# Optimization experiments

Measured on AMD Instinct MI355X. Metric: run time of the kernel, lower is better.

Reference implementation:

```python
import jax, jax.numpy as jnp
import numpy as np

EPS = 1e-4  # performer softmax-kernel stabilizer
LN_EPS = 1e-5


def _layernorm(x, g, b):
    m = jnp.mean(x, axis=-1, keepdims=True)
    v = jnp.mean(jnp.square(x - m), axis=-1, keepdims=True)
    return (x - m) * jax.lax.rsqrt(v + LN_EPS) * g + b


def _softmax_features(x, proj, is_query):
    # FAVOR+ positive softmax-kernel features. x: [B,H,N,Dh], proj: [M,Dh]
    d = x.shape[-1]
    xn = x * (d ** -0.25)                      # data normalizer d^{-1/4}
    u = jnp.einsum('bhnd,md->bhnm', xn, proj)  # [B,H,N,M]
    diag = 0.5 * jnp.sum(jnp.square(xn), axis=-1, keepdims=True)
    if is_query:
        stab = jnp.max(u, axis=-1, keepdims=True)
    else:
        stab = jnp.max(u, axis=(-2, -1), keepdims=True)
    ratio = proj.shape[0] ** -0.5
    return ratio * (jnp.exp(u - diag - stab) + EPS)


def reference(x, proj, ln1_g, ln1_b, ln2_g, ln2_b, W1, b1, W2, b2):
    B, N, E = x.shape
    M, Dh = proj.shape
    H = E // Dh

    # --- multi-head fast attention sublayer (pre-LN, q=k=v, no dropout) ---
    h = _layernorm(x, ln1_g, ln1_b)
    qkv = h.reshape(B, N, H, Dh).transpose(0, 2, 1, 3)     # [B,H,N,Dh]
    q_p = _softmax_features(qkv, proj, is_query=True)      # [B,H,N,M]
    k_p = _softmax_features(qkv, proj, is_query=False)     # [B,H,N,M]

    # non-causal linear attention: O(N*M*Dh)
    k_sum = jnp.sum(k_p, axis=-2)                          # [B,H,M]
    d_inv = 1.0 / jnp.einsum('bhnm,bhm->bhn', q_p, k_sum)  # [B,H,N]
    ctx = jnp.einsum('bhnm,bhnd->bhmd', k_p, qkv)          # [B,H,M,Dh]
    attn = jnp.einsum('bhnm,bhmd,bhn->bhnd', q_p, ctx, d_inv)
    attn = attn.transpose(0, 2, 1, 3).reshape(B, N, E)
    x = x + attn

    # --- MLP sublayer (pre-LN, GELU, dropout off in eval) ---
    h2 = _layernorm(x, ln2_g, ln2_b)
    h2 = jax.nn.gelu(h2 @ W1 + b1, approximate=False) @ W2 + b2
    return x + h2


def setup_inputs() -> dict:
    B, N, E, H, M, F = 4, 2048, 768, 12, 256, 3072
    Dh = E // H
    key = jax.random.key(0)
    ks = jax.random.split(key, 4)
    return {
        'x': jax.random.normal(ks[0], (B, N, E), jnp.float32),
        'proj': jax.random.normal(ks[1], (M, Dh), jnp.float32),
        'ln1_g': jnp.ones((E,), jnp.float32),
        'ln1_b': jnp.zeros((E,), jnp.float32),
        'ln2_g': jnp.ones((E,), jnp.float32),
        'ln2_b': jnp.zeros((E,), jnp.float32),
        'W1': jax.random.normal(ks[2], (E, F), jnp.float32) * 0.02,
        'b1': jnp.zeros((F,), jnp.float32),
        'W2': jax.random.normal(ks[3], (F, E), jnp.float32) * 0.02,
        'b2': jnp.zeros((E,), jnp.float32),
    }
```

## Files before the change

### kernel.cpp

```cpp
#include <hip/hip_runtime.h>
#include <hip/hip_bf16.h>
#include <math.h>

#define B_    4
#define N_    2048
#define E_    768
#define H_    12
#define M_    256
#define F_    3072
#define DH_   64
#define BN_   (B_ * N_)
#define BH_   (B_ * H_)
#define NSP_  16

#define EPS_F     1e-4f
#define LN_EPS_F  1e-5f
#define DNORM_F   0.35355339059327373f
#define DIAGC_F   0.0625f

typedef __attribute__((ext_vector_type(8))) short bf16x8;
typedef __attribute__((ext_vector_type(4))) float f32x4;

static __device__ __forceinline__ float to_f32(float v) { return v; }
static __device__ __forceinline__ float to_f32(__hip_bfloat16 v) { return __bfloat162float(v); }
static __device__ __forceinline__ short f2bf(float v) {
    __hip_bfloat16 b = __float2bfloat16(v);
    return *reinterpret_cast<short*>(&b);
}

static __device__ __forceinline__ float fast_gelu(float x) {
    float xc = fminf(fmaxf(x, -9.f), 9.f);
    float y = 0.7978845608028654f * (xc + 0.044715f * xc * xc * xc);
    float tt = __expf(-2.f * y);
    return x * __builtin_amdgcn_rcpf(1.f + tt);
}

static __device__ __forceinline__ void gld_lds16(const void* g, void* lds) {
    __builtin_amdgcn_global_load_lds((const __attribute__((address_space(1))) void*)g,
                                     (__attribute__((address_space(3))) void*)lds, 16, 0, 0);
}

__global__ void probe_kernel(const unsigned int* __restrict__ g1, int* __restrict__ flag) {
    if (threadIdx.x == 0 && blockIdx.x == 0)
        *flag = (*g1 == 0x3F803F80u) ? 1 : 0;
}

__global__ void convert_kernel(const void* __restrict__ src, __hip_bfloat16* __restrict__ dst,
                               int n, const int* __restrict__ flag) {
    int isb = *flag;
    int i = blockIdx.x * blockDim.x + threadIdx.x;
    int stride = gridDim.x * blockDim.x;
    if (isb) {
        const unsigned short* s = (const unsigned short*)src;
        unsigned short* d = (unsigned short*)dst;
        for (; i < n; i += stride) d[i] = s[i];
    } else {
        const float* s = (const float*)src;
        for (; i < n; i += stride) dst[i] = __float2bfloat16(s[i]);
    }
}

__global__ void convert_transpose_kernel(const void* __restrict__ src,
                                         __hip_bfloat16* __restrict__ dst,
                                         int R, int C, const int* __restrict__ flag) {
    __shared__ __hip_bfloat16 tile[32][33];
    int isb = *flag;
    int c0 = blockIdx.x * 32, r0 = blockIdx.y * 32;
    int tx = threadIdx.x & 31, ty = threadIdx.x >> 5;
    if (isb) {
        const unsigned short* s = (const unsigned short*)src;
        for (int j = 0; j < 4; ++j) {
            int r = ty + j * 8;
            ((unsigned short*)&tile[r][tx])[0] = s[(size_t)(r0 + r) * C + c0 + tx];
        }
    } else {
        const float* s = (const float*)src;
        for (int j = 0; j < 4; ++j) {
            int r = ty + j * 8;
            tile[r][tx] = __float2bfloat16(s[(size_t)(r0 + r) * C + c0 + tx]);
        }
    }
    __syncthreads();
    for (int j = 0; j < 4; ++j) {
        int r = ty + j * 8;
        dst[(size_t)(c0 + r) * R + r0 + tx] = tile[tx][r];
    }
}

template <typename TIn>
__global__ void ln_kernel(const TIn* __restrict__ x,
                          const __hip_bfloat16* __restrict__ g,
                          const __hip_bfloat16* __restrict__ b,
                          __hip_bfloat16* __restrict__ hout,
                          float* __restrict__ diag ) {
    int row = blockIdx.x;
    int t = threadIdx.x;
    __shared__ float rs[256], rq[256];
    __shared__ float hrow[E_];

    float xv[3];
    const TIn* xr = x + (size_t)row * E_;
    float s = 0.f, q = 0.f;
    for (int i = 0; i < 3; ++i) {
        xv[i] = to_f32(xr[t + i * 256]);
        s += xv[i];
        q += xv[i] * xv[i];
    }
    rs[t] = s; rq[t] = q;
    __syncthreads();
    for (int off = 128; off > 0; off >>= 1) {
        if (t < off) { rs[t] += rs[t + off]; rq[t] += rq[t + off]; }
        __syncthreads();
    }
    float mean = rs[0] * (1.0f / E_);
    float var  = rq[0] * (1.0f / E_) - mean * mean;
    float rinv = rsqrtf(fmaxf(var, 0.0f) + LN_EPS_F);

    __hip_bfloat16* hr = hout + (size_t)row * E_;
    for (int i = 0; i < 3; ++i) {
        int e = t + i * 256;
        float hv = (xv[i] - mean) * rinv * __bfloat162float(g[e]) + __bfloat162float(b[e]);
        hr[e] = __float2bfloat16(hv);
        hrow[e] = hv;
    }
    if (diag != nullptr) {
        __syncthreads();
        if (t < H_) {
            float acc = 0.f;
            for (int k = 0; k < DH_; ++k) { float v = hrow[t * DH_ + k]; acc += v * v; }
            diag[row * H_ + t] = DIAGC_F * acc;
        }
    }
}

__global__ __launch_bounds__(256) void ctx_mfma_kernel(
        const __hip_bfloat16* __restrict__ h,
        const __hip_bfloat16* __restrict__ proj,
        const float* __restrict__ diag,
        float* __restrict__ pctx, float* __restrict__ pksum,
        float* __restrict__ pmax, float* __restrict__ pvsum) {
    int sp = blockIdx.x, bh = blockIdx.y;
    int bb = bh / H_, hh = bh % H_;
    int n0 = sp * 128;
    int t = threadIdx.x, lane = t & 63, w = t >> 6;
    int lm = lane & 15, kg = lane >> 4;

    __shared__ __align__(16) short hv_s[128 * 72];
    __shared__ __align__(16) short vt_s[64 * 136];
    __shared__ __align__(16) short p_s[64 * 72];
    __shared__ __align__(16) short kpt_s[64 * 136];
    __shared__ float ksp_s[4][64];
    __shared__ float dg_s[128];
    __shared__ float wmax_s[4];
    __shared__ float vp_s[4][64];

    for (int it = 0; it < 4; ++it) {
        int c = t + it * 256; int n = c >> 3, kb = c & 7;
        uint4 vld = *(const uint4*)&h[((size_t)(bb * N_ + n0 + n)) * E_ + hh * DH_ + kb * 8];
        *(uint4*)&hv_s[n * 72 + kb * 8] = vld;
        union { uint4 u4; short sh[8]; } uu; uu.u4 = vld;
        for (int j = 0; j < 8; ++j) vt_s[(kb * 8 + j) * 136 + n] = uu.sh[j];
    }
    if (t < 128) dg_s[t] = diag[(size_t)(bb * N_ + n0 + t) * H_ + hh];
    __syncthreads();

    {
        int d = t & 63, rg = t >> 6;
        float s = 0.f;
        for (int n = rg * 32; n < rg * 32 + 32; ++n)
            s += __bfloat162float(*(const __hip_bfloat16*)&hv_s[n * 72 + d]);
        vp_s[rg][d] = s;
    }
    __syncthreads();
    if (t < 64)
        pvsum[((size_t)sp * BH_ + bh) * 64 + t] =
            vp_s[0][t] + vp_s[1][t] + vp_s[2][t] + vp_s[3][t];

    for (int q = 0; q < 4; ++q) {
        __syncthreads();
        for (int it = 0; it < 2; ++it) {
            int c = t + it * 256; int m = c >> 3, kb = c & 7;
            *(uint4*)&p_s[m * 72 + kb * 8] = *(const uint4*)&proj[(size_t)(q * 64 + m) * DH_ + kb * 8];
        }
        __syncthreads();

        f32x4 u[2][4];
        for (int i = 0; i < 2; ++i) for (int j = 0; j < 4; ++j) u[i][j] = (f32x4){0.f,0.f,0.f,0.f};
        for (int kc = 0; kc < 2; ++kc) {
            bf16x8 af[2], bf[4];
            for (int i = 0; i < 2; ++i)
                af[i] = *(const bf16x8*)&hv_s[(w * 32 + i * 16 + lm) * 72 + kc * 32 + kg * 8];
            for (int j = 0; j < 4; ++j)
                bf[j] = *(const bf16x8*)&p_s[(j * 16 + lm) * 72 + kc * 32 + kg * 8];
            for (int i = 0; i < 2; ++i)
                for (int j = 0; j < 4; ++j)
                    u[i][j] = __builtin_amdgcn_mfma_f32_16x16x32_bf16(af[i], bf[j], u[i][j], 0, 0, 0);
        }
        float lmax = -1e30f;
        for (int i = 0; i < 2; ++i) for (int j = 0; j < 4; ++j) for (int r = 0; r < 4; ++r) {
            u[i][j][r] *= DNORM_F;
            lmax = fmaxf(lmax, u[i][j][r]);
        }
        for (int off = 32; off >= 1; off >>= 1) lmax = fmaxf(lmax, __shfl_xor(lmax, off));
        if (lane == 0) wmax_s[w] = lmax;
        __syncthreads();
        float Lmax = fmaxf(fmaxf(wmax_s[0], wmax_s[1]), fmaxf(wmax_s[2], wmax_s[3]));

        float kpart[4] = {0.f, 0.f, 0.f, 0.f};
        for (int i = 0; i < 2; ++i) {
            float dgv[4];
            for (int r = 0; r < 4; ++r) dgv[r] = dg_s[w * 32 + i * 16 + kg * 4 + r];
            for (int j = 0; j < 4; ++j)
                for (int r = 0; r < 4; ++r) {
                    float val = expf(u[i][j][r] - dgv[r] - Lmax);
                    kpart[j] += val;
                    kpt_s[(j * 16 + lm) * 136 + (w * 32 + i * 16 + kg * 4 + r)] = f2bf(val);
                }
        }
        for (int j = 0; j < 4; ++j) {
            kpart[j] += __shfl_xor(kpart[j], 16);
            kpart[j] += __shfl_xor(kpart[j], 32);
        }
        if (lane < 16)
            for (int j = 0; j < 4; ++j) ksp_s[w][j * 16 + lm] = kpart[j];
        __syncthreads();

        f32x4 c4[4];
        for (int jd = 0; jd < 4; ++jd) c4[jd] = (f32x4){0.f,0.f,0.f,0.f};
        for (int kc = 0; kc < 4; ++kc) {
            bf16x8 a = *(const bf16x8*)&kpt_s[(w * 16 + lm) * 136 + kc * 32 + kg * 8];
            for (int jd = 0; jd < 4; ++jd) {
                bf16x8 b = *(const bf16x8*)&vt_s[(jd * 16 + lm) * 136 + kc * 32 + kg * 8];
                c4[jd] = __builtin_amdgcn_mfma_f32_16x16x32_bf16(a, b, c4[jd], 0, 0, 0);
            }
        }
        size_t base = ((size_t)sp * BH_ + bh) * M_ + q * 64 + w * 16;
        for (int jd = 0; jd < 4; ++jd)
            for (int r = 0; r < 4; ++r)
                pctx[(base + kg * 4 + r) * DH_ + jd * 16 + lm] = c4[jd][r];
        if (t < 64)
            pksum[((size_t)sp * BH_ + bh) * M_ + q * 64 + t] =
                ksp_s[0][t] + ksp_s[1][t] + ksp_s[2][t] + ksp_s[3][t];
        if (t == 0) pmax[bh * 64 + sp * 4 + q] = Lmax;
    }
}

__global__ void ctx_reduce_kernel(const float* __restrict__ pctx,
                                  const float* __restrict__ pksum,
                                  const float* __restrict__ pmax,
                                  const float* __restrict__ pvsum,
                                  __hip_bfloat16* __restrict__ ctx_t,
                                  float* __restrict__ ksum) {
    int mb = blockIdx.x, bh = blockIdx.y;
    int t = threadIdx.x;
    __shared__ float hm_s;
    __shared__ float sc_s[16];
    __shared__ float vs_s[64];
    __shared__ float tr_s[64 * 65];
    if (t < 64) {
        float v = pmax[bh * 64 + t];
        for (int off = 32; off >= 1; off >>= 1) v = fmaxf(v, __shfl_xor(v, off));
        if (t == 0) hm_s = v;
        float s = 0.f;
        for (int sp = 0; sp < 16; ++sp) s += pvsum[((size_t)sp * BH_ + bh) * 64 + t];
        vs_s[t] = s;
    }
    __syncthreads();
    if (t < 16) sc_s[t] = expf(pmax[bh * 64 + t * 4 + mb] - hm_s);
    __syncthreads();
    float scl[16];
    for (int sp = 0; sp < 16; ++sp) scl[sp] = sc_s[sp];
    int d = t & 63;
    for (int it = 0; it < 16; ++it) {
        int ml = (t >> 6) + it * 4;
        float acc = 0.f;
        for (int sp = 0; sp < 16; ++sp)
            acc += scl[sp] * pctx[(((size_t)sp * BH_ + bh) * M_ + mb * 64 + ml) * DH_ + d];
        tr_s[ml * 65 + d] = acc + EPS_F * vs_s[d];
    }
    if (t < 64) {
        float ka = 0.f;
        for (int sp = 0; sp < 16; ++sp)
            ka += scl[sp] * pksum[((size_t)sp * BH_ + bh) * M_ + mb * 64 + t];
        ksum[bh * M_ + mb * 64 + t] = ka + EPS_F * (float)N_;
    }
    __syncthreads();
    int mcol = t & 63;
    for (int jt = 0; jt < 16; ++jt) {
        int dl = (t >> 6) + jt * 4;
        ctx_t[((size_t)bh * DH_ + dl) * M_ + mb * 64 + mcol] = __float2bfloat16(tr_s[mcol * 65 + dl]);
    }
}

__global__ void sums_kernel(const __hip_bfloat16* __restrict__ ctx_t,
                            const float* __restrict__ ksum,
                            float* __restrict__ ctxsum, float* __restrict__ kssum) {
    int bh = blockIdx.x, t = threadIdx.x;
    __shared__ float red[256];
    int d = t >> 2, part = t & 3;
    float s = 0.f;
    for (int mm = part * 64; mm < part * 64 + 64; ++mm)
        s += __bfloat162float(ctx_t[((size_t)bh * DH_ + d) * M_ + mm]);
    red[t] = s;
    __syncthreads();
    if (t < 64) ctxsum[bh * 64 + t] = red[t * 4] + red[t * 4 + 1] + red[t * 4 + 2] + red[t * 4 + 3];
    __syncthreads();
    red[t] = ksum[bh * M_ + t];
    __syncthreads();
    for (int off = 128; off > 0; off >>= 1) {
        if (t < off) red[t] += red[t + off];
        __syncthreads();
    }
    if (t == 0) kssum[bh] = red[0];
}

__global__ __launch_bounds__(256) void attn_mfma_kernel(
        const __hip_bfloat16* __restrict__ h,
        const __hip_bfloat16* __restrict__ proj,
        const float* __restrict__ diag,
        const __hip_bfloat16* __restrict__ ctx_t,
        const float* __restrict__ ksum,
        const float* __restrict__ ctxsum,
        const float* __restrict__ kssum,
        const __hip_bfloat16* __restrict__ xin,
        float* __restrict__ x2) {
    int ntile = blockIdx.x, bh = blockIdx.y;
    int bb = bh / H_, hh = bh % H_;
    int n0 = ntile * 128;
    int t = threadIdx.x, lane = t & 63, w = t >> 6;
    int lm = lane & 15, kg = lane >> 4;

    __shared__ __align__(16) short hq_s[128 * 72];
    __shared__ __align__(16) short p_s[64 * 72];
    __shared__ __align__(16) short ct_s[64 * 72];
    __shared__ __align__(16) short qp_s[128 * 72];
    __shared__ float ksum_s[256];
    __shared__ float dg_s[128];
    __shared__ float cs_s[64];
    __shared__ float kss_s;

    for (int it = 0; it < 4; ++it) {
        int c = t + it * 256; int n = c >> 3, kb = c & 7;
        *(uint4*)&hq_s[n * 72 + kb * 8] =
            *(const uint4*)&h[((size_t)(bb * N_ + n0 + n)) * E_ + hh * DH_ + kb * 8];
    }
    if (t < 128) dg_s[t] = diag[(size_t)(bb * N_ + n0 + t) * H_ + hh];
    ksum_s[t] = ksum[bh * M_ + t];
    if (t < 64) cs_s[t] = ctxsum[bh * 64 + t];
    if (t == 0) kss_s = kssum[bh];

    f32x4 o[2][4];
    float qs[2][4], mrun[2][4];
    for (int i = 0; i < 2; ++i)
        for (int jd = 0; jd < 4; ++jd) o[i][jd] = (f32x4){0.f,0.f,0.f,0.f};
    for (int i = 0; i < 2; ++i)
        for (int r = 0; r < 4; ++r) { qs[i][r] = 0.f; mrun[i][r] = -1e30f; }

    for (int mc = 0; mc < 4; ++mc) {
        __syncthreads();
        for (int it = 0; it < 2; ++it) {
            int c = t + it * 256; int m = c >> 3, kb = c & 7;
            *(uint4*)&p_s[m * 72 + kb * 8] = *(const uint4*)&proj[(size_t)(mc * 64 + m) * DH_ + kb * 8];
            *(uint4*)&ct_s[m * 72 + kb * 8] =
                *(const uint4*)&ctx_t[((size_t)bh * DH_ + m) * M_ + mc * 64 + kb * 8];
        }
        __syncthreads();

        f32x4 u[2][4];
        for (int i = 0; i < 2; ++i) for (int j = 0; j < 4; ++j) u[i][j] = (f32x4){0.f,0.f,0.f,0.f};
        for (int kc = 0; kc < 2; ++kc) {
            bf16x8 af[2], bf[4];
            for (int i = 0; i < 2; ++i)
                af[i] = *(const bf16x8*)&hq_s[(w * 32 + i * 16 + lm) * 72 + kc * 32 + kg * 8];
            for (int j = 0; j < 4; ++j)
                bf[j] = *(const bf16x8*)&p_s[(j * 16 + lm) * 72 + kc * 32 + kg * 8];
            for (int i = 0; i < 2; ++i)
                for (int j = 0; j < 4; ++j)
                    u[i][j] = __builtin_amdgcn_mfma_f32_16x16x32_bf16(af[i], bf[j], u[i][j], 0, 0, 0);
        }
        for (int i = 0; i < 2; ++i) for (int j = 0; j < 4; ++j)
            for (int r = 0; r < 4; ++r) u[i][j][r] *= DNORM_F;

        for (int i = 0; i < 2; ++i)
            for (int r = 0; r < 4; ++r) {
                float cm = fmaxf(fmaxf(u[i][0][r], u[i][1][r]), fmaxf(u[i][2][r], u[i][3][r]));
                for (int off = 8; off >= 1; off >>= 1) cm = fmaxf(cm, __shfl_xor(cm, off));
                float mnew = fmaxf(mrun[i][r], cm);
                float sc = expf(mrun[i][r] - mnew);
                mrun[i][r] = mnew;
                qs[i][r] *= sc;
                for (int jd = 0; jd < 4; ++jd) o[i][jd][r] *= sc;
            }
        for (int i = 0; i < 2; ++i) {
            float dgv[4];
            for (int r = 0; r < 4; ++r) dgv[r] = dg_s[w * 32 + i * 16 + kg * 4 + r];
            for (int j = 0; j < 4; ++j) {
                float ksv = ksum_s[mc * 64 + j * 16 + lm];
                for (int r = 0; r < 4; ++r) {
                    float val = expf(u[i][j][r] - dgv[r] - mrun[i][r]);
                    qs[i][r] += val * ksv;
                    qp_s[(w * 32 + i * 16 + kg * 4 + r) * 72 + j * 16 + lm] = f2bf(val);
                }
            }
        }
        __syncthreads();
        for (int kc = 0; kc < 2; ++kc) {
            bf16x8 af[2], bf[4];
            for (int i = 0; i < 2; ++i)
                af[i] = *(const bf16x8*)&qp_s[(w * 32 + i * 16 + lm) * 72 + kc * 32 + kg * 8];
            for (int jd = 0; jd < 4; ++jd)
                bf[jd] = *(const bf16x8*)&ct_s[(jd * 16 + lm) * 72 + kc * 32 + kg * 8];
            for (int i = 0; i < 2; ++i)
                for (int jd = 0; jd < 4; ++jd)
                    o[i][jd] = __builtin_amdgcn_mfma_f32_16x16x32_bf16(af[i], bf[jd], o[i][jd], 0, 0, 0);
        }
    }

    for (int i = 0; i < 2; ++i)
        for (int r = 0; r < 4; ++r)
            for (int off = 8; off >= 1; off >>= 1) qs[i][r] += __shfl_xor(qs[i][r], off);
    float kss = kss_s;
    for (int i = 0; i < 2; ++i)
        for (int r = 0; r < 4; ++r) {
            float dinv = 1.0f / (qs[i][r] + EPS_F * kss);
            size_t row = (size_t)(bb * N_ + n0 + w * 32 + i * 16 + kg * 4 + r);
            for (int jd = 0; jd < 4; ++jd) {
                int dcol = jd * 16 + lm;
                float outv = (o[i][jd][r] + EPS_F * cs_s[dcol]) * dinv;
                int col = hh * DH_ + dcol;
                x2[row * E_ + col] = __bfloat162float(xin[row * E_ + col]) + outv;
            }
        }
}

template <int KK, int NCOLS, bool DO_GELU>
__global__ __launch_bounds__(256, 2) void mfma_mlp_kernel(
        const __hip_bfloat16* __restrict__ A,
        const __hip_bfloat16* __restrict__ Bt,
        const __hip_bfloat16* __restrict__ bias,
        const float* __restrict__ resid,
        void* __restrict__ outv,
        const int* __restrict__ oflag) {
    constexpr int TM = 128, TN = 128;
    constexpr int CA = TM / 16;
    constexpr int CPS = CA + TN / 16;
    constexpr int CPW = CPS / 4;
    constexpr int LBUF = CPS * 512;
    constexpr int NT = KK / 32;
    constexpr int NXB = NCOLS / TN;
    constexpr int NWG = NXB * (BN_ / TM);
    constexpr int CPX = NWG / 8;

    const int t = threadIdx.x;
    const int bid0 = blockIdx.y * NXB + blockIdx.x;
    const int bid = (bid0 & 7) * CPX + (bid0 >> 3);
    const int col0 = (bid % NXB) * TN;
    const int row0 = (bid / NXB) * TM;

    const int lane = t & 63, w = t >> 6;
    const int wr = w & 1, wc = w >> 1;
    const int lm = lane & 15, kg = lane >> 4;
    const int lp = lane ^ ((lane >> 3) & 7);
    const int lr = lp >> 2, lc = (lp & 3) * 8;
    const int sxa = (lm >> 1) << 3;

    __shared__ __align__(16) short Ls[2 * LBUF];

    const __hip_bfloat16* gp[CPW];
    int lof[CPW];
#pragma unroll
    for (int cc = 0; cc < CPW; ++cc) {
        int c = w + cc * 4;
        gp[cc] = (c < CA) ? &A[(size_t)(row0 + c * 16 + lr) * KK + lc]
                          : &Bt[(size_t)(col0 + (c - CA) * 16 + lr) * KK + lc];
        lof[cc] = c * 512;
    }

    f32x4 acc[4][4];
#pragma unroll
    for (int i = 0; i < 4; ++i)
#pragma unroll
        for (int j = 0; j < 4; ++j)
            acc[i][j] = (f32x4){0.f, 0.f, 0.f, 0.f};

#pragma unroll
    for (int cc = 0; cc < CPW; ++cc) gld_lds16(gp[cc], &Ls[lof[cc]]);

    int cur = 0;
    for (int ts = 0; ts < NT; ++ts) {
        if (ts + 1 < NT) {
            const int nb = (cur ^ 1) * LBUF;
            const int ko = (ts + 1) * 32;
#pragma unroll
            for (int cc = 0; cc < CPW; ++cc)
                gld_lds16(gp[cc] + ko, &Ls[nb + lof[cc]]);
            asm volatile("s_waitcnt vmcnt(%0)" :: "n"(CPW) : "memory");
        } else {
            asm volatile("s_waitcnt vmcnt(0)" ::: "memory");
        }
        __builtin_amdgcn_s_barrier();

        const short* base = &Ls[cur * LBUF];
        bf16x8 af[4], bfr[4];
#pragma unroll
        for (int i = 0; i < 4; ++i)
            af[i] = *(const bf16x8*)&base[(wr * 4 + i) * 512 + ((lm * 32 + kg * 8) ^ sxa)];
#pragma unroll
        for (int j = 0; j < 4; ++j)
            bfr[j] = *(const bf16x8*)&base[(CA + wc * 4 + j) * 512 + ((lm * 32 + kg * 8) ^ sxa)];

        asm volatile("s_waitcnt lgkmcnt(0)" ::: "memory");
        __builtin_amdgcn_sched_barrier(0);
        __builtin_amdgcn_s_barrier();

#pragma unroll
        for (int i = 0; i < 4; ++i)
#pragma unroll
            for (int j = 0; j < 4; ++j)
                acc[i][j] = __builtin_amdgcn_mfma_f32_16x16x32_bf16(af[i], bfr[j], acc[i][j], 0, 0, 0);
        cur ^= 1;
    }

    int ob = DO_GELU ? 1 : *oflag;
#pragma unroll
    for (int i = 0; i < 4; ++i) {
#pragma unroll
        for (int r = 0; r < 4; ++r) {
            int row = row0 + wr * 64 + i * 16 + kg * 4 + r;
            size_t rb = (size_t)row * NCOLS;
#pragma unroll
            for (int j = 0; j < 4; ++j) {
                int col = col0 + wc * 64 + j * 16 + lm;
                float v = acc[i][j][r] + __bfloat162float(bias[col]);
                if (DO_GELU) {
                    v = fast_gelu(v);
                } else {
                    v += resid[rb + col];
                }
                if (ob) ((__hip_bfloat16*)outv)[rb + col] = __float2bfloat16(v);
                else    ((float*)outv)[rb + col] = v;
            }
        }
    }
}

extern "C" void kernel_launch(void* const* d_in, const int* in_sizes, int n_in,
                              void* d_out, int out_size, void* d_ws, size_t ws_size,
                              hipStream_t stream) {
    char* ws = (char*)d_ws;
    size_t off = 0;
    auto carve = [&](size_t bytes) -> void* {
        void* p = ws + off;
        off += (bytes + 255) & ~(size_t)255;
        return p;
    };
    float*          x2    = (float*)carve((size_t)BN_ * E_ * 4);
    __hip_bfloat16* h     = (__hip_bfloat16*)carve((size_t)BN_ * E_ * 2);
    __hip_bfloat16* Wt1   = (__hip_bfloat16*)carve((size_t)E_ * F_ * 2);
    __hip_bfloat16* Wt2   = (__hip_bfloat16*)carve((size_t)F_ * E_ * 2);
    __hip_bfloat16* projc = (__hip_bfloat16*)carve((size_t)M_ * DH_ * 2);
    __hip_bfloat16* g1c   = (__hip_bfloat16*)carve((size_t)E_ * 2);
    __hip_bfloat16* b1lc  = (__hip_bfloat16*)carve((size_t)E_ * 2);
    __hip_bfloat16* g2c   = (__hip_bfloat16*)carve((size_t)E_ * 2);
    __hip_bfloat16* b2lc  = (__hip_bfloat16*)carve((size_t)E_ * 2);
    __hip_bfloat16* bb1c  = (__hip_bfloat16*)carve((size_t)F_ * 2);
    __hip_bfloat16* bb2c  = (__hip_bfloat16*)carve((size_t)E_ * 2);
    int*            flag  = (int*)carve(256);
    size_t mark = off;
    __hip_bfloat16* xc    = (__hip_bfloat16*)carve((size_t)BN_ * E_ * 2);
    float*          diag  = (float*)carve((size_t)BN_ * H_ * 4);
    float*          pctx  = (float*)carve((size_t)NSP_ * BH_ * M_ * DH_ * 4);
    float*          pksum = (float*)carve((size_t)NSP_ * BH_ * M_ * 4);
    float*          pmax  = (float*)carve((size_t)BH_ * 64 * 4);
    float*          pvsum = (float*)carve((size_t)NSP_ * BH_ * 64 * 4);
    __hip_bfloat16* ctx_t = (__hip_bfloat16*)carve((size_t)BH_ * DH_ * M_ * 2);
    float*          ksum  = (float*)carve((size_t)BH_ * M_ * 4);
    float*          ctxsum= (float*)carve((size_t)BH_ * DH_ * 4);
    float*          kssum = (float*)carve((size_t)BH_ * 4);
    __hip_bfloat16* h2    = h;
    __hip_bfloat16* mid   = (__hip_bfloat16*)(ws + mark);

    probe_kernel<<<1, 64, 0, stream>>>((const unsigned int*)d_in[2], flag);
    struct { const void* src; __hip_bfloat16* dst; int n; } cv[8] = {
        { d_in[0], xc,    BN_ * E_ },
        { d_in[1], projc, M_ * DH_ },
        { d_in[2], g1c,   E_ },
        { d_in[3], b1lc,  E_ },
        { d_in[4], g2c,   E_ },
        { d_in[5], b2lc,  E_ },
        { d_in[7], bb1c,  F_ },
        { d_in[9], bb2c,  E_ },
    };
    for (int i = 0; i < 8; ++i) {
        int blocks = (cv[i].n + 255) / 256; if (blocks > 1024) blocks = 1024;
        convert_kernel<<<blocks, 256, 0, stream>>>(cv[i].src, cv[i].dst, cv[i].n, flag);
    }
    convert_transpose_kernel<<<dim3(F_ / 32, E_ / 32), 256, 0, stream>>>(d_in[6], Wt1, E_, F_, flag);
    convert_transpose_kernel<<<dim3(E_ / 32, F_ / 32), 256, 0, stream>>>(d_in[8], Wt2, F_, E_, flag);

    ln_kernel<__hip_bfloat16><<<BN_, 256, 0, stream>>>(xc, g1c, b1lc, h, diag);
    ctx_mfma_kernel<<<dim3(NSP_, BH_), 256, 0, stream>>>(h, projc, diag, pctx, pksum, pmax, pvsum);
    ctx_reduce_kernel<<<dim3(4, BH_), 256, 0, stream>>>(pctx, pksum, pmax, pvsum, ctx_t, ksum);
    sums_kernel<<<BH_, 256, 0, stream>>>(ctx_t, ksum, ctxsum, kssum);
    attn_mfma_kernel<<<dim3(16, BH_), 256, 0, stream>>>(h, projc, diag, ctx_t, ksum, ctxsum, kssum, xc, x2);

    ln_kernel<float><<<BN_, 256, 0, stream>>>(x2, g2c, b2lc, h2, nullptr);
    mfma_mlp_kernel<E_, F_, true><<<dim3(F_ / 128, BN_ / 128), 256, 0, stream>>>(
        h2, Wt1, bb1c, nullptr, (void*)mid, flag);
    mfma_mlp_kernel<F_, E_, false><<<dim3(E_ / 128, BN_ / 128), 256, 0, stream>>>(
        mid, Wt2, bb2c, x2, d_out, flag);
}
```

Measured before the change: 376.2 us.

## Add triple-buffered LDS pipeline with register prefetch for second MLP GEMM

Adds a PIPE template variant of the MLP GEMM that uses three LDS buffers, issuing global loads two k-steps ahead. It also double-buffers the MFMA operand fragments in registers, so the LDS reads for the next step overlap the current MFMAs. Only the second GEMM (K=3072, N=768) uses it; the first keeps the old double-buffered loop. The cost is more LDS and more VGPRs, which could lower occupancy under launch_bounds(256,2) or cause spills.

```diff
diff --git a/kernel.cpp b/kernel.cpp
--- a/kernel.cpp
+++ b/kernel.cpp
@@ -433,7 +433,7 @@
         }
 }
 
-template <int KK, int NCOLS, bool DO_GELU>
+template <int KK, int NCOLS, int PIPE, bool DO_GELU>
 __global__ __launch_bounds__(256, 2) void mfma_mlp_kernel(
         const __hip_bfloat16* __restrict__ A,
         const __hip_bfloat16* __restrict__ Bt,
@@ -446,6 +446,7 @@
     constexpr int CPS = CA + TN / 16;
     constexpr int CPW = CPS / 4;
     constexpr int LBUF = CPS * 512;
+    constexpr int NBUF = (PIPE == 1) ? 3 : 2;
     constexpr int NT = KK / 32;
     constexpr int NXB = NCOLS / TN;
     constexpr int NWG = NXB * (BN_ / TM);
@@ -464,7 +465,7 @@
     const int lr = lp >> 2, lc = (lp & 3) * 8;
     const int sxa = (lm >> 1) << 3;
 
-    __shared__ __align__(16) short Ls[2 * LBUF];
+    __shared__ __align__(16) short Ls[NBUF * LBUF];
 
     const __hip_bfloat16* gp[CPW];
     int lof[CPW];
@@ -483,42 +484,99 @@
         for (int j = 0; j < 4; ++j)
             acc[i][j] = (f32x4){0.f, 0.f, 0.f, 0.f};
 
-#pragma unroll
-    for (int cc = 0; cc < CPW; ++cc) gld_lds16(gp[cc], &Ls[lof[cc]]);
-
-    int cur = 0;
-    for (int ts = 0; ts < NT; ++ts) {
-        if (ts + 1 < NT) {
-            const int nb = (cur ^ 1) * LBUF;
-            const int ko = (ts + 1) * 32;
-#pragma unroll
-            for (int cc = 0; cc < CPW; ++cc)
-                gld_lds16(gp[cc] + ko, &Ls[nb + lof[cc]]);
-            asm volatile("s_waitcnt vmcnt(%0)" :: "n"(CPW) : "memory");
-        } else {
-            asm volatile("s_waitcnt vmcnt(0)" ::: "memory");
-        }
+    const int fro = (lm * 32 + kg * 8) ^ sxa;
+
+    if constexpr (PIPE == 0) {
+#pragma unroll
+        for (int cc = 0; cc < CPW; ++cc) gld_lds16(gp[cc], &Ls[lof[cc]]);
+        int cur = 0;
+        for (int ts = 0; ts < NT; ++ts) {
+            if (ts + 1 < NT) {
+                const int nb = (cur ^ 1) * LBUF;
+                const int ko = (ts + 1) * 32;
+#pragma unroll
+                for (int cc = 0; cc < CPW; ++cc)
+                    gld_lds16(gp[cc] + ko, &Ls[nb + lof[cc]]);
+                asm volatile("s_waitcnt vmcnt(%0)" :: "n"(CPW) : "memory");
+            } else {
+                asm volatile("s_waitcnt vmcnt(0)" ::: "memory");
+            }
+            __builtin_amdgcn_s_barrier();
+
+            const short* base = &Ls[cur * LBUF];
+            bf16x8 af[4], bfr[4];
+#pragma unroll
+            for (int i = 0; i < 4; ++i)
+                af[i] = *(const bf16x8*)&base[(wr * 4 + i) * 512 + fro];
+#pragma unroll
+            for (int j = 0; j < 4; ++j)
+                bfr[j] = *(const bf16x8*)&base[(CA + wc * 4 + j) * 512 + fro];
+
+            asm volatile("s_waitcnt lgkmcnt(0)" ::: "memory");
+            __builtin_amdgcn_sched_barrier(0);
+            __builtin_amdgcn_s_barrier();
+
+#pragma unroll
+            for (int i = 0; i < 4; ++i)
+#pragma unroll
+                for (int j = 0; j < 4; ++j)
+                    acc[i][j] = __builtin_amdgcn_mfma_f32_16x16x32_bf16(af[i], bfr[j], acc[i][j], 0, 0, 0);
+            cur ^= 1;
+        }
+    } else {
+        bf16x8 fA[8], fB[8];
+        int cur = 0;
+#pragma unroll
+        for (int cc = 0; cc < CPW; ++cc) gld_lds16(gp[cc], &Ls[lof[cc]]);
+#pragma unroll
+        for (int cc = 0; cc < CPW; ++cc) gld_lds16(gp[cc] + 32, &Ls[LBUF + lof[cc]]);
+        asm volatile("s_waitcnt vmcnt(%0)" :: "n"(CPW) : "memory");
         __builtin_amdgcn_s_barrier();
-
-        const short* base = &Ls[cur * LBUF];
-        bf16x8 af[4], bfr[4];
 #pragma unroll
         for (int i = 0; i < 4; ++i)
-            af[i] = *(const bf16x8*)&base[(wr * 4 + i) * 512 + ((lm * 32 + kg * 8) ^ sxa)];
+            fA[i] = *(const bf16x8*)&Ls[(wr * 4 + i) * 512 + fro];
 #pragma unroll
         for (int j = 0; j < 4; ++j)
-            bfr[j] = *(const bf16x8*)&base[(CA + wc * 4 + j) * 512 + ((lm * 32 + kg * 8) ^ sxa)];
-
-        asm volatile("s_waitcnt lgkmcnt(0)" ::: "memory");
-        __builtin_amdgcn_sched_barrier(0);
-        __builtin_amdgcn_s_barrier();
-
-#pragma unroll
-        for (int i = 0; i < 4; ++i)
-#pragma unroll
-            for (int j = 0; j < 4; ++j)
-                acc[i][j] = __builtin_amdgcn_mfma_f32_16x16x32_bf16(af[i], bfr[j], acc[i][j], 0, 0, 0);
-        cur ^= 1;
+            fA[4 + j] = *(const bf16x8*)&Ls[(CA + wc * 4 + j) * 512 + fro];
+
+        auto step = [&](int ts, bf16x8 (&FC)[8], bf16x8 (&FN)[8]) {
+            const int nxt = (cur + 1 == 3) ? 0 : cur + 1;
+            const int nb  = (cur + 2 >= 3) ? cur - 1 : cur + 2;
+            if (ts + 2 < NT) {
+                const int ko = (ts + 2) * 32;
+#pragma unroll
+                for (int cc = 0; cc < CPW; ++cc)
+                    gld_lds16(gp[cc] + ko, &Ls[nb * LBUF + lof[cc]]);
+                asm volatile("s_waitcnt vmcnt(%0)" :: "n"(CPW) : "memory");
+            } else if (ts + 1 < NT) {
+                asm volatile("s_waitcnt vmcnt(0)" ::: "memory");
+            }
+            __builtin_amdgcn_s_barrier();
+            if (ts + 1 < NT) {
+                const short* nbase = &Ls[nxt * LBUF];
+#pragma unroll
+                for (int i = 0; i < 4; ++i)
+                    FN[i] = *(const bf16x8*)&nbase[(wr * 4 + i) * 512 + fro];
+#pragma unroll
+                for (int j = 0; j < 4; ++j)
+                    FN[4 + j] = *(const bf16x8*)&nbase[(CA + wc * 4 + j) * 512 + fro];
+                asm volatile("s_waitcnt lgkmcnt(8)" ::: "memory");
+            } else {
+                asm volatile("s_waitcnt lgkmcnt(0)" ::: "memory");
+            }
+            __builtin_amdgcn_sched_barrier(0);
+#pragma unroll
+            for (int i = 0; i < 4; ++i)
+#pragma unroll
+                for (int j = 0; j < 4; ++j)
+                    acc[i][j] = __builtin_amdgcn_mfma_f32_16x16x32_bf16(FC[i], FC[4 + j], acc[i][j], 0, 0, 0);
+            if (ts + 1 < NT) __builtin_amdgcn_s_barrier();
+            cur = nxt;
+        };
+        for (int ts = 0; ts < NT; ts += 2) {
+            step(ts, fA, fB);
+            step(ts + 1, fB, fA);
+        }
     }
 
     int ob = DO_GELU ? 1 : *oflag;
@@ -605,8 +663,8 @@
     attn_mfma_kernel<<<dim3(16, BH_), 256, 0, stream>>>(h, projc, diag, ctx_t, ksum, ctxsum, kssum, xc, x2);
 
     ln_kernel<float><<<BN_, 256, 0, stream>>>(x2, g2c, b2lc, h2, nullptr);
-    mfma_mlp_kernel<E_, F_, true><<<dim3(F_ / 128, BN_ / 128), 256, 0, stream>>>(
+    mfma_mlp_kernel<E_, F_, 0, true><<<dim3(F_ / 128, BN_ / 128), 256, 0, stream>>>(
         h2, Wt1, bb1c, nullptr, (void*)mid, flag);
-    mfma_mlp_kernel<F_, E_, false><<<dim3(E_ / 128, BN_ / 128), 256, 0, stream>>>(
+    mfma_mlp_kernel<F_, E_, 1, false><<<dim3(E_ / 128, BN_ / 128), 256, 0, stream>>>(
         mid, Wt2, bb2c, x2, d_out, flag);
 }
```

Result: no change. 378.1 us (+0.5%).
